# Kernel optimization log

Hardware: AMD Instinct MI355X
Metric: run time of the kernel (lower is better)

Reference implementation:

```python
import jax, jax.numpy as jnp
import numpy as np

B, S, HID = 1, 2048, 2048
H, KVH, D, VD = 32, 8, 128, 128
R = 64  # rope_dim = head_dim * partial_rotary_factor, rounded down to even
N_REP = H // KVH
SCALE = D ** -0.5
NEG = -1e9


def _rotate_half(x):
    half = x.shape[-1] // 2
    return jnp.concatenate([-x[..., half:], x[..., :half]], axis=-1)


def setup_inputs() -> dict:
    key = jax.random.key(0)
    ks = jax.random.split(key, 8)
    hidden_states = jax.random.normal(ks[0], (B, S, HID), dtype=jnp.float32)
    # RoPE angles: standard inverse-frequency positional embedding of width R
    inv_freq = 1.0 / (10000.0 ** (np.arange(0, R, 2, dtype=np.float32) / R))
    pos = np.arange(S, dtype=np.float32)
    freqs = np.outer(pos, inv_freq)                       # [S, R/2]
    emb = np.concatenate([freqs, freqs], axis=-1)         # [S, R]
    cos = jnp.asarray(np.cos(emb))[None].repeat(B, axis=0)  # [B, S, R]
    sin = jnp.asarray(np.sin(emb))[None].repeat(B, axis=0)
    # additive causal mask [B, 1, S, S]
    causal = jnp.triu(jnp.full((S, S), NEG, dtype=jnp.float32), k=1)
    attention_mask = jnp.broadcast_to(causal[None, None], (B, 1, S, S))
    std = 0.02
    Wq = jax.random.normal(ks[1], (H * D, HID), dtype=jnp.float32) * std
    Wk = jax.random.normal(ks[2], (KVH * D, HID), dtype=jnp.float32) * std
    Wv = jax.random.normal(ks[3], (KVH * VD, HID), dtype=jnp.float32) * std
    Wo = jax.random.normal(ks[4], (HID, H * VD), dtype=jnp.float32) * std
    sink_bias = jax.random.normal(ks[5], (H,), dtype=jnp.float32) * 0.5
    return {"hidden_states": hidden_states, "cos": cos, "sin": sin,
            "attention_mask": attention_mask, "Wq": Wq, "Wk": Wk, "Wv": Wv,
            "Wo": Wo, "sink_bias": sink_bias}


def reference(hidden_states, cos, sin, attention_mask, Wq, Wk, Wv, Wo, sink_bias):
    b, s, _ = hidden_states.shape
    # projections -> [B, heads, S, dim]
    q = (hidden_states @ Wq.T).reshape(b, s, H, D).transpose(0, 2, 1, 3)
    k = (hidden_states @ Wk.T).reshape(b, s, KVH, D).transpose(0, 2, 1, 3)
    v = (hidden_states @ Wv.T).reshape(b, s, KVH, VD).transpose(0, 2, 1, 3)
    # partial RoPE on first R dims
    c = cos[:, None, :, :]  # [B,1,S,R]
    si = sin[:, None, :, :]
    q_r, q_n = q[..., :R], q[..., R:]
    k_r, k_n = k[..., :R], k[..., R:]
    q = jnp.concatenate([q_r * c + _rotate_half(q_r) * si, q_n], axis=-1)
    k = jnp.concatenate([k_r * c + _rotate_half(k_r) * si, k_n], axis=-1)
    # GQA: repeat kv heads
    k_rep = jnp.repeat(k, N_REP, axis=1)
    v_rep = jnp.repeat(v, N_REP, axis=1)
    scores = jnp.einsum('bhqd,bhkd->bhqk', q, k_rep) * SCALE + attention_mask
    # extra attention-sink logit column per head
    sinks = jnp.broadcast_to(sink_bias.reshape(1, H, 1, 1), (b, H, s, 1))
    aw = jnp.concatenate([scores, sinks], axis=-1)            # [B,H,S,S+1]
    probs = jax.nn.softmax(aw, axis=-1)[..., :-1]             # drop sink column
    out = jnp.einsum('bhqk,bhkd->bhqd', probs, v_rep)
    out = out.transpose(0, 2, 1, 3).reshape(b, s, H * VD)
    return out @ Wo.T
```

## Files before the change

### kernel.cpp

```cpp
#include <hip/hip_runtime.h>

typedef unsigned short u16;
typedef unsigned int   u32;
typedef __bf16  bf16x8 __attribute__((ext_vector_type(8)));
typedef float   f32x4  __attribute__((ext_vector_type(4)));
typedef float   f32x16 __attribute__((ext_vector_type(16)));
typedef u16     u16x4  __attribute__((ext_vector_type(4)));
typedef u16     u16x8  __attribute__((ext_vector_type(8)));
typedef u32     u32x4  __attribute__((ext_vector_type(4)));

#define S_LEN 2048
#define NH 32
#define NKVH 8
#define HD 128
#define QKVST 6144
#define AOST  4096
#define ATT_SCALE 0.08838834764831845f
#define LOG2E 1.4426950408889634f
#define QSC2 (ATT_SCALE * LOG2E)
#define RESCALE_THR2 11.5f

__device__ __forceinline__ u16 f2bf(float f){
  u32 u = __builtin_bit_cast(u32, f);
  u += 0x7FFFu + ((u >> 16) & 1u);
  return (u16)(u >> 16);
}
__device__ __forceinline__ u32 cvtpk(float lo, float hi){
  u32 d;
  asm("v_cvt_pk_bf16_f32 %0, %1, %2" : "=v"(d) : "v"(lo), "v"(hi));
  return d;
}
__device__ __forceinline__ void gload_lds16(const u16* g, u16* l){
  __builtin_amdgcn_global_load_lds(
      (const __attribute__((address_space(1))) void*)g,
      (__attribute__((address_space(3))) void*)l, 16, 0, 0);
}

__global__ void cvt_all_kernel(const f32x4* __restrict__ hs, const f32x4* __restrict__ wq,
                               const f32x4* __restrict__ wk, const f32x4* __restrict__ wv,
                               const f32x4* __restrict__ wo, u16x4* __restrict__ out){
  int i = blockIdx.x * 256 + threadIdx.x;
  const f32x4* src; int off;
  if      (i < 1048576){ src = hs; off = i; }
  else if (i < 3145728){ src = wq; off = i - 1048576; }
  else if (i < 3670016){ src = wk; off = i - 3145728; }
  else if (i < 4194304){ src = wv; off = i - 3670016; }
  else                 { src = wo; off = i - 4194304; }
  f32x4 v = src[off];
  u16x4 o;
  o[0] = f2bf(v[0]); o[1] = f2bf(v[1]); o[2] = f2bf(v[2]); o[3] = f2bf(v[3]);
  out[i] = o;
}

template<int OUT_BF16, int ROPE, int BM, int BN>
__global__ __launch_bounds__(256, 2)
void gemm_bt_kernel(const u16* __restrict__ X, const u16* __restrict__ W,
                    void* __restrict__ Cv, int M, int N, int K,
                    const float* __restrict__ cosv, const float* __restrict__ sinv){
  __shared__ __align__(16) u16 As[2][2][BM * 32];
  __shared__ __align__(16) u16 Bs[2][2][BN * 32];
  const int MI = BM / 32, NJ = BN / 32;
  const int m0 = blockIdx.y * BM, n0 = blockIdx.x * BN;
  const int tid = threadIdx.x;
  const int wave = tid >> 6, lane = tid & 63;
  const int wm = wave >> 1, wn = wave & 1;
  const int g = lane >> 4, ln = lane & 15;
  const int r0 = tid >> 2;
  const int cc = (tid & 3) * 8;
  f32x4 acc[MI][NJ] = {};
  const u16* xa0 = X + (size_t)(m0 + r0) * K + cc;
  const u16* xa1 = X + (size_t)(m0 + r0 + 64) * K + cc;
  const u16* wb0 = W + (size_t)(n0 + r0) * K + cc;
  const u16* wb1 = W + (size_t)(n0 + r0 + 64) * K + cc;

  auto stage = [&](int buf, int k0){
    #pragma unroll
    for (int s = 0; s < 2; s++){
      const int kc = k0 + s * 32;
      gload_lds16(xa0 + kc, &As[buf][s][tid * 8]);
      if (BM == 128) gload_lds16(xa1 + kc, &As[buf][s][2048 + tid * 8]);
      gload_lds16(wb0 + kc, &Bs[buf][s][tid * 8]);
      if (BN == 128) gload_lds16(wb1 + kc, &Bs[buf][s][2048 + tid * 8]);
    }
  };

  stage(0, 0);
  __syncthreads();
  int cur = 0;
  for (int k0 = 0; k0 < K; k0 += 64){
    if (k0 + 64 < K) stage(cur ^ 1, k0 + 64);
    #pragma unroll
    for (int s = 0; s < 2; s++){
      bf16x8 a[MI], b[NJ];
      #pragma unroll
      for (int f = 0; f < MI; f++) a[f] = *(const bf16x8*)&As[cur][s][(wm * (BM / 2) + f * 16 + ln) * 32 + g * 8];
      #pragma unroll
      for (int f = 0; f < NJ; f++) b[f] = *(const bf16x8*)&Bs[cur][s][(wn * (BN / 2) + f * 16 + ln) * 32 + g * 8];
      __builtin_amdgcn_s_setprio(1);
      #pragma unroll
      for (int i = 0; i < MI; i++)
        #pragma unroll
        for (int j = 0; j < NJ; j++)
          acc[i][j] = __builtin_amdgcn_mfma_f32_16x16x32_bf16(a[i], b[j], acc[i][j], 0, 0, 0);
      __builtin_amdgcn_s_setprio(0);
    }
    __syncthreads();
    cur ^= 1;
  }
  if (ROPE && BN == 128){
    if (wn == 0 && n0 < 5120){
      #pragma unroll
      for (int i = 0; i < MI; i++)
        #pragma unroll
        for (int r = 0; r < 4; r++){
          const int row = m0 + wm * (BM / 2) + i * 16 + g * 4 + r;
          #pragma unroll
          for (int j = 0; j < 2; j++){
            const int d = j * 16 + ln;
            float c  = cosv[row * 64 + d];
            float sn = sinv[row * 64 + d];
            float x0 = acc[i][j][r], x1 = acc[i][j + 2][r];
            acc[i][j][r]     = x0 * c - x1 * sn;
            acc[i][j + 2][r] = x1 * c + x0 * sn;
          }
        }
    }
    if (n0 < 4096){
      #pragma unroll
      for (int i = 0; i < MI; i++)
        #pragma unroll
        for (int j = 0; j < NJ; j++)
          #pragma unroll
          for (int r = 0; r < 4; r++) acc[i][j][r] *= QSC2;
    }
  }
  #pragma unroll
  for (int i = 0; i < MI; i++)
    #pragma unroll
    for (int j = 0; j < NJ; j++)
      #pragma unroll
      for (int r = 0; r < 4; r++){
        int row = m0 + wm * (BM / 2) + i * 16 + g * 4 + r;
        int col = n0 + wn * (BN / 2) + j * 16 + ln;
        if (OUT_BF16) ((u16*)Cv)[(size_t)row * N + col] = f2bf(acc[i][j][r]);
        else          ((float*)Cv)[(size_t)row * N + col] = acc[i][j][r];
      }
}

__global__ void vtrans_kernel(const u16* __restrict__ QKV, u16* __restrict__ VT){
  int idx = blockIdx.x * 256 + threadIdx.x;
  if (idx >= NKVH * HD * S_LEN) return;
  int s   = idx & (S_LEN - 1);
  int vd  = (idx >> 11) & (HD - 1);
  int kvh = idx >> 18;
  VT[idx] = QKV[(size_t)s * QKVST + 5120 + kvh * HD + vd];
}

__global__ __launch_bounds__(256, 2)
void attn_kernel(const u16* __restrict__ QKV, const u16* __restrict__ VT,
                 const float* __restrict__ sinkb, u16* __restrict__ AO){
  __shared__ __align__(16) u16 Ks[2][32 * 256];
  __shared__ __align__(16) u16 Vs[2][32 * 256];
  const int b    = blockIdx.x;
  const int kvh  = b & 7;
  const int head = kvh * 4 + ((b >> 3) & 3);
  const int slot = b >> 5;
  const int qt   = (slot < 8) ? (15 - slot) : (slot - 8);
  const int tid  = threadIdx.x;
  const int w    = tid >> 6;
  const int lane = tid & 63;
  const int l31  = lane & 31, hi = lane >> 5;
  const int q0   = qt * 128;
  const int qw   = q0 + w * 32;

  const u16* Kbase = QKV + 4096 + kvh * HD;
  const u16* Vbase = VT + (size_t)kvh * HD * S_LEN;

  auto stage = [&](int buf, int kt){
    const int k0 = kt * 64;
    #pragma unroll
    for (int p = 0; p < 4; p++){
      int idx = p * 256 + tid;
      int r = idx >> 5, c = idx & 31;
      int cs = c ^ r;
      int key = r * 2 + (cs >> 4), d8 = (cs & 15) * 8;
      gload_lds16(Kbase + (size_t)(k0 + key) * QKVST + d8, &Ks[buf][idx * 8]);
    }
    #pragma unroll
    for (int p = 0; p < 4; p++){
      int idx = p * 256 + tid;
      int r = idx >> 5, c = idx & 31;
      int cs = c ^ r;
      int vd = r * 4 + (cs >> 3), k8 = (cs & 7) * 8;
      gload_lds16(Vbase + (size_t)vd * S_LEN + k0 + k8, &Vs[buf][idx * 8]);
    }
  };

  bf16x8 qB[8];
  const u16* qrow = QKV + (size_t)(qw + l31) * QKVST + head * HD;
  #pragma unroll
  for (int t = 0; t < 8; t++) qB[t] = *(const bf16x8*)(qrow + t * 16 + hi * 8);

  float m  = sinkb[head] * LOG2E;
  float Ll = (hi == 0) ? 1.f : 0.f;
  f32x16 O[4] = {};

  const int nkt = 2 * qt + 2;
  stage(0, 0);
  __syncthreads();
  int cur = 0;

  for (int kt = 0; kt < nkt; kt++){
    const int k0 = kt * 64;
    if (kt + 1 < nkt) stage(cur ^ 1, kt + 1);

    if (k0 < qw + 32){
      const u16* Kc = Ks[cur];
      const u16* Vc = Vs[cur];
      f32x16 sc0 = {}, sc1 = {};
      const int krow0 = (l31 >> 1);
      const int kc0   = ((l31 & 1) << 4) | hi;
      __builtin_amdgcn_s_setprio(1);
      #pragma unroll
      for (int t = 0; t < 8; t++){
        bf16x8 ka0 = *(const bf16x8*)&Kc[krow0 * 256 + ((kc0 + 2 * t) ^ krow0) * 8];
        bf16x8 ka1 = *(const bf16x8*)&Kc[(16 + krow0) * 256 + ((kc0 + 2 * t) ^ (16 + krow0)) * 8];
        sc0 = __builtin_amdgcn_mfma_f32_32x32x16_bf16(ka0, qB[t], sc0, 0, 0, 0);
        sc1 = __builtin_amdgcn_mfma_f32_32x32x16_bf16(ka1, qB[t], sc1, 0, 0, 0);
      }
      __builtin_amdgcn_s_setprio(0);

      if (k0 + 63 > qw){
        const int qg = qw + l31;
        #pragma unroll
        for (int r = 0; r < 16; r++){
          int keyr = k0 + (r & 3) + 8 * (r >> 2) + 4 * hi;
          if (keyr      > qg) sc0[r] = -1e30f;
          if (keyr + 32 > qg) sc1[r] = -1e30f;
        }
      }
      float mx = sc0[0];
      #pragma unroll
      for (int r = 1; r < 16; r++) mx = fmaxf(mx, sc0[r]);
      #pragma unroll
      for (int r = 0; r < 16; r++) mx = fmaxf(mx, sc1[r]);
      mx = fmaxf(mx, __shfl_xor(mx, 32));
      if (!__all(mx <= m + RESCALE_THR2)){
        float mn = fmaxf(m, mx);
        float sf = exp2f(m - mn);
        m = mn;
        #pragma unroll
        for (int n = 0; n < 4; n++)
          #pragma unroll
          for (int r = 0; r < 16; r++) O[n][r] *= sf;
        Ll *= sf;
      }
      float p0[16], p1[16];
      #pragma unroll
      for (int r = 0; r < 16; r++){ p0[r] = exp2f(sc0[r] - m); Ll += p0[r]; }
      #pragma unroll
      for (int r = 0; r < 16; r++){ p1[r] = exp2f(sc1[r] - m); Ll += p1[r]; }

      __builtin_amdgcn_s_setprio(1);
      #pragma unroll
      for (int c = 0; c < 4; c++){
        const float* ps = (c & 2) ? p1 : p0;
        const int bb = (c & 1) * 8;
        u32 wa = cvtpk(ps[bb + 0], ps[bb + 1]);
        u32 wb = cvtpk(ps[bb + 2], ps[bb + 3]);
        u32 wc = cvtpk(ps[bb + 4], ps[bb + 5]);
        u32 wd = cvtpk(ps[bb + 6], ps[bb + 7]);
        asm("v_permlane32_swap_b32 %0, %1" : "+v"(wa), "+v"(wc));
        asm("v_permlane32_swap_b32 %0, %1" : "+v"(wb), "+v"(wd));
        u32x4 wv_; wv_[0] = wa; wv_[1] = wb; wv_[2] = wc; wv_[3] = wd;
        bf16x8 pf = __builtin_bit_cast(bf16x8, wv_);
        #pragma unroll
        for (int n = 0; n < 4; n++){
          const int vrow = n * 8 + (l31 >> 2);
          const int vcc  = ((l31 & 3) << 3) | (c << 1) | hi;
          bf16x8 va = *(const bf16x8*)&Vc[vrow * 256 + (vcc ^ vrow) * 8];
          O[n] = __builtin_amdgcn_mfma_f32_32x32x16_bf16(va, pf, O[n], 0, 0, 0);
        }
      }
      __builtin_amdgcn_s_setprio(0);
    }
    __syncthreads();
    cur ^= 1;
  }

  float l = Ll + __shfl_xor(Ll, 32);
  float inv = 1.f / l;
  u16* arena = &Ks[0][0];
  #pragma unroll
  for (int n = 0; n < 4; n++)
    #pragma unroll
    for (int r = 0; r < 16; r++){
      int vd = n * 32 + (r & 3) + 8 * (r >> 2) + 4 * hi;
      int ch = (vd >> 3) ^ (l31 & 15);
      arena[w * 4096 + l31 * 128 + ch * 8 + (vd & 7)] = f2bf(O[n][r] * inv);
    }
  __syncthreads();
  #pragma unroll
  for (int p = 0; p < 8; p++){
    int idx = p * 256 + tid;
    int row = idx >> 4, c = idx & 15;
    u16x8 v = *(const u16x8*)&arena[row * 128 + ((c ^ (row & 15)) * 8)];
    *(u16x8*)&AO[(size_t)(q0 + row) * AOST + head * HD + c * 8] = v;
  }
}

extern "C" void kernel_launch(void* const* d_in, const int* in_sizes, int n_in,
                              void* d_out, int out_size, void* d_ws, size_t ws_size,
                              hipStream_t stream){
  (void)in_sizes; (void)n_in; (void)out_size; (void)ws_size;
  const float* hs    = (const float*)d_in[0];
  const float* cosv  = (const float*)d_in[1];
  const float* sinv  = (const float*)d_in[2];
  const float* Wq    = (const float*)d_in[4];
  const float* Wk    = (const float*)d_in[5];
  const float* Wv    = (const float*)d_in[6];
  const float* Wo    = (const float*)d_in[7];
  const float* sinkb = (const float*)d_in[8];
  float* out = (float*)d_out;

  char* ws = (char*)d_ws;
  u16* XB    = (u16*)(ws);
  u16* WQKVB = (u16*)(ws + 8388608);
  u16* WOB   = (u16*)(ws + 33554432);
  u16* QKV   = (u16*)(ws + 50331648);
  u16* VT    = (u16*)(ws + 75497472);
  u16* AO    = (u16*)(ws + 79691776);

  cvt_all_kernel<<<24576, 256, 0, stream>>>((const f32x4*)hs, (const f32x4*)Wq,
                                            (const f32x4*)Wk, (const f32x4*)Wv,
                                            (const f32x4*)Wo, (u16x4*)ws);

  gemm_bt_kernel<1, 1, 64, 128><<<dim3(48, 32), 256, 0, stream>>>(XB, WQKVB, QKV, 2048, 6144, 2048, cosv, sinv);

  vtrans_kernel<<<8192, 256, 0, stream>>>(QKV, VT);

  attn_kernel<<<dim3(512), 256, 0, stream>>>(QKV, VT, sinkb, AO);

  gemm_bt_kernel<0, 0, 128, 64><<<dim3(32, 16), 256, 0, stream>>>(AO, WOB, out, 2048, 2048, 4096, nullptr, nullptr);
}
```

Baseline: 239.1 us.

## Share K/V tiles across the four GQA query heads in one attention block

The attention kernel is restructured so each 512-thread block handles one KV head and a 64-row query tile for all four query heads sharing that KV head. Previously each block handled one query head with 128 query rows. Each staged K/V tile is now reused by four heads, which cuts global-to-LDS traffic per unit of work, and blocks are ordered longest-first. The row-max reduction is also rewritten as a tree to shorten the dependency chain. Costs: the grid shrinks to 256 blocks, blocks are larger, and causal load balance changes.

```diff
diff --git a/kernel.cpp b/kernel.cpp
--- a/kernel.cpp
+++ b/kernel.cpp
@@ -156,22 +156,20 @@
   VT[idx] = QKV[(size_t)s * QKVST + 5120 + kvh * HD + vd];
 }
 
-__global__ __launch_bounds__(256, 2)
+__global__ __launch_bounds__(512, 2)
 void attn_kernel(const u16* __restrict__ QKV, const u16* __restrict__ VT,
                  const float* __restrict__ sinkb, u16* __restrict__ AO){
-  __shared__ __align__(16) u16 Ks[2][32 * 256];
-  __shared__ __align__(16) u16 Vs[2][32 * 256];
+  __shared__ __align__(16) u16 lds[4][32 * 256];
   const int b    = blockIdx.x;
   const int kvh  = b & 7;
-  const int head = kvh * 4 + ((b >> 3) & 3);
-  const int slot = b >> 5;
-  const int qt   = (slot < 8) ? (15 - slot) : (slot - 8);
+  const int qt   = 31 - (b >> 3);
   const int tid  = threadIdx.x;
   const int w    = tid >> 6;
+  const int head = kvh * 4 + (w >> 1);
   const int lane = tid & 63;
   const int l31  = lane & 31, hi = lane >> 5;
-  const int q0   = qt * 128;
-  const int qw   = q0 + w * 32;
+  const int q0   = qt * 64;
+  const int qw   = q0 + (w & 1) * 32;
 
   const u16* Kbase = QKV + 4096 + kvh * HD;
   const u16* Vbase = VT + (size_t)kvh * HD * S_LEN;
@@ -179,20 +177,20 @@
   auto stage = [&](int buf, int kt){
     const int k0 = kt * 64;
     #pragma unroll
-    for (int p = 0; p < 4; p++){
-      int idx = p * 256 + tid;
+    for (int p = 0; p < 2; p++){
+      int idx = p * 512 + tid;
       int r = idx >> 5, c = idx & 31;
       int cs = c ^ r;
       int key = r * 2 + (cs >> 4), d8 = (cs & 15) * 8;
-      gload_lds16(Kbase + (size_t)(k0 + key) * QKVST + d8, &Ks[buf][idx * 8]);
-    }
-    #pragma unroll
-    for (int p = 0; p < 4; p++){
-      int idx = p * 256 + tid;
+      gload_lds16(Kbase + (size_t)(k0 + key) * QKVST + d8, &lds[buf][idx * 8]);
+    }
+    #pragma unroll
+    for (int p = 0; p < 2; p++){
+      int idx = p * 512 + tid;
       int r = idx >> 5, c = idx & 31;
       int cs = c ^ r;
       int vd = r * 4 + (cs >> 3), k8 = (cs & 7) * 8;
-      gload_lds16(Vbase + (size_t)vd * S_LEN + k0 + k8, &Vs[buf][idx * 8]);
+      gload_lds16(Vbase + (size_t)vd * S_LEN + k0 + k8, &lds[2 + buf][idx * 8]);
     }
   };
 
@@ -205,7 +203,7 @@
   float Ll = (hi == 0) ? 1.f : 0.f;
   f32x16 O[4] = {};
 
-  const int nkt = 2 * qt + 2;
+  const int nkt = qt + 1;
   stage(0, 0);
   __syncthreads();
   int cur = 0;
@@ -215,8 +213,8 @@
     if (kt + 1 < nkt) stage(cur ^ 1, kt + 1);
 
     if (k0 < qw + 32){
-      const u16* Kc = Ks[cur];
-      const u16* Vc = Vs[cur];
+      const u16* Kc = lds[cur];
+      const u16* Vc = lds[2 + cur];
       f32x16 sc0 = {}, sc1 = {};
       const int krow0 = (l31 >> 1);
       const int kc0   = ((l31 & 1) << 4) | hi;
@@ -239,11 +237,14 @@
           if (keyr + 32 > qg) sc1[r] = -1e30f;
         }
       }
-      float mx = sc0[0];
-      #pragma unroll
-      for (int r = 1; r < 16; r++) mx = fmaxf(mx, sc0[r]);
-      #pragma unroll
-      for (int r = 0; r < 16; r++) mx = fmaxf(mx, sc1[r]);
+      float m4[4];
+      #pragma unroll
+      for (int j = 0; j < 4; j++){
+        float a = fmaxf(fmaxf(sc0[j*4], sc0[j*4+1]), fmaxf(sc0[j*4+2], sc0[j*4+3]));
+        float c = fmaxf(fmaxf(sc1[j*4], sc1[j*4+1]), fmaxf(sc1[j*4+2], sc1[j*4+3]));
+        m4[j] = fmaxf(a, c);
+      }
+      float mx = fmaxf(fmaxf(m4[0], m4[1]), fmaxf(m4[2], m4[3]));
       mx = fmaxf(mx, __shfl_xor(mx, 32));
       if (!__all(mx <= m + RESCALE_THR2)){
         float mn = fmaxf(m, mx);
@@ -290,22 +291,23 @@
 
   float l = Ll + __shfl_xor(Ll, 32);
   float inv = 1.f / l;
-  u16* arena = &Ks[0][0];
+  u16* arena = &lds[0][0];
+  const int rr = w * 32 + l31;
   #pragma unroll
   for (int n = 0; n < 4; n++)
     #pragma unroll
     for (int r = 0; r < 16; r++){
       int vd = n * 32 + (r & 3) + 8 * (r >> 2) + 4 * hi;
       int ch = (vd >> 3) ^ (l31 & 15);
-      arena[w * 4096 + l31 * 128 + ch * 8 + (vd & 7)] = f2bf(O[n][r] * inv);
+      arena[rr * 128 + ch * 8 + (vd & 7)] = f2bf(O[n][r] * inv);
     }
   __syncthreads();
   #pragma unroll
   for (int p = 0; p < 8; p++){
-    int idx = p * 256 + tid;
+    int idx = p * 512 + tid;
     int row = idx >> 4, c = idx & 15;
     u16x8 v = *(const u16x8*)&arena[row * 128 + ((c ^ (row & 15)) * 8)];
-    *(u16x8*)&AO[(size_t)(q0 + row) * AOST + head * HD + c * 8] = v;
+    *(u16x8*)&AO[(size_t)(q0 + (row & 63)) * AOST + (kvh * 4 + (row >> 6)) * HD + c * 8] = v;
   }
 }
 
@@ -339,7 +341,7 @@
 
   vtrans_kernel<<<8192, 256, 0, stream>>>(QKV, VT);
 
-  attn_kernel<<<dim3(512), 256, 0, stream>>>(QKV, VT, sinkb, AO);
+  attn_kernel<<<dim3(256), 512, 0, stream>>>(QKV, VT, sinkb, AO);
 
   gemm_bt_kernel<0, 0, 128, 64><<<dim3(32, 16), 256, 0, stream>>>(AO, WOB, out, 2048, 2048, 4096, nullptr, nullptr);
 }
```

Result: slower. 246.2 us (+3.0%).
